# Kernel optimization log

Hardware: AMD Instinct MI355X
Metric: run time of the kernel (lower is better)

The kernel has to match this reference:

```python
import jax, jax.numpy as jnp
import numpy as np

HIDDEN = 768
NUM_LABELS = 25


def setup_inputs() -> dict:
    key = jax.random.key(0)
    k1, k2, k3, k4, k5 = jax.random.split(key, 5)
    B, H, S, E = 2, 12, 256, 64
    attention_probs = jax.random.uniform(k1, (B, H, S, S), dtype=jnp.float32)
    value_attentions = jax.random.normal(k2, (B, H, S, E), dtype=jnp.float32)
    relative_positions = jax.random.normal(k3, (B, S, S, H * E), dtype=jnp.float32)
    # nn.Linear(hidden_size, num_labels): weight [L, hidden], bias [L]
    bound = 1.0 / np.sqrt(HIDDEN)
    W = jax.random.uniform(k4, (NUM_LABELS, HIDDEN), dtype=jnp.float32, minval=-bound, maxval=bound)
    b = jax.random.uniform(k5, (NUM_LABELS,), dtype=jnp.float32, minval=-bound, maxval=bound)
    return {
        "attention_probs": attention_probs,
        "value_attentions": value_attentions,
        "relative_positions": relative_positions,
        "W": W,
        "b": b,
    }


def reference(attention_probs, value_attentions, relative_positions, W, b):
    B, H, S, E = value_attentions.shape
    # out[b,h,i,j,e] = probs[b,h,i,j] * (value[b,h,j,e] + rel[b,h,i,j,e])
    p = attention_probs[..., None]                      # [B,H,S,S,1]
    v = value_attentions[:, :, None, :, :]              # [B,H,1,S,E] broadcast over i
    rel = relative_positions.reshape(B, S, S, H, E).transpose(0, 3, 1, 2, 4)  # [B,H,S,S,E]
    out = p * (v + rel)                                 # [B,H,i,j,E]
    # permute(0,3,2,1,4) -> [B, j, i, H, E] -> [B,S,S,H*E]
    out = out.transpose(0, 3, 2, 1, 4).reshape(B, S, S, H * E)
    out = out @ W.T + b                                 # [B,S,S,L]
    return out.transpose(0, 1, 3, 2)                    # [B,S,L,S]
```

## Files before the change

### kernel.cpp

```cpp
#include <hip/hip_runtime.h>

#define NB 2
#define NH 12
#define NS 256
#define NE 64
#define NC 768
#define NL 25

__global__ __launch_bounds__(256) void tmhs_main(
    const float* __restrict__ p,
    const float* __restrict__ v,
    const float* __restrict__ rel,
    const float* __restrict__ W,
    const float* __restrict__ bias,
    float* __restrict__ out)
{
    __shared__ float sR[64][68];

    const int tid = threadIdx.x;
    const int bx  = blockIdx.x;
    const int it  = bx & 3;
    const int j   = (bx >> 2) & 255;
    const int b   = bx >> 10;
    const int i0  = it << 6;

    const int ig = tid & 63;
    const int wv = __builtin_amdgcn_readfirstlane(tid >> 6);
    const int l0 = wv * 6;

    float acc[7] = {0.f,0.f,0.f,0.f,0.f,0.f,0.f};

    const int row  = tid >> 2;
    const int part = tid & 3;

    for (int k = 0; k < NH; ++k) {
        __syncthreads();
        {
            const float  pr = p[((b*NH + k)*NS + (i0 + row))*NS + j];
            const float4* vp = (const float4*)(v + (((b*NH + k)*NS + j) << 6) + part*16);
            const float4* rs = (const float4*)(rel + ((b*NS + (i0+row))*NS + j)*NC + k*64 + part*16);
            float4* dst = (float4*)&sR[row][part*16];
#pragma unroll
            for (int q = 0; q < 4; ++q) {
                float4 a = rs[q];
                const float4 bb = vp[q];
                a.x = pr*(a.x + bb.x); a.y = pr*(a.y + bb.y);
                a.z = pr*(a.z + bb.z); a.w = pr*(a.w + bb.w);
                dst[q] = a;
            }
        }
        __syncthreads();

        const float* wk = W + k*64;
#pragma unroll
        for (int e4 = 0; e4 < 16; ++e4) {
            const float4 r4 = *(const float4*)&sR[ig][e4*4];
#pragma unroll
            for (int u = 0; u < 7; ++u) {
                const float4 w4 = *(const float4*)(wk + (l0 + u)*NC + e4*4);
                acc[u] = fmaf(r4.x, w4.x, acc[u]);
                acc[u] = fmaf(r4.y, w4.y, acc[u]);
                acc[u] = fmaf(r4.z, w4.z, acc[u]);
                acc[u] = fmaf(r4.w, w4.w, acc[u]);
            }
        }
    }

    const int ob = ((b*NS + j)*NL)*NS + i0 + ig;
#pragma unroll
    for (int u = 0; u < 7; ++u) {
        const int l = l0 + u;
        out[ob + l*NS] = acc[u] + bias[l];
    }
}

extern "C" void kernel_launch(void* const* d_in, const int* in_sizes, int n_in,
                              void* d_out, int out_size, void* d_ws, size_t ws_size,
                              hipStream_t stream) {
    const float* p    = (const float*)d_in[0];
    const float* v    = (const float*)d_in[1];
    const float* rel  = (const float*)d_in[2];
    const float* W    = (const float*)d_in[3];
    const float* bias = (const float*)d_in[4];
    float* out = (float*)d_out;
    tmhs_main<<<dim3(NB * NS * 4), dim3(256), 0, stream>>>(p, v, rel, W, bias, out);
}
```

Before: 612.0 us.

## Use bf16 MFMA for the label projection with a padded bf16 weight copy

Replaces the scalar FP32 FMA projection with bf16 MFMA 16x16x32 instructions. W is first converted to a zero-padded 32-row bf16 buffer in workspace by a separate prep kernel. The fused activations are packed to bf16 in shared memory, and the tiling changes to 128 i-rows per block over 128-wide K chunks. The kernel is dominated by the large rel stream, so compute savings may matter less, and bf16 lowers accuracy.

```diff
diff --git a/kernel.cpp b/kernel.cpp
--- a/kernel.cpp
+++ b/kernel.cpp
@@ -1,4 +1,5 @@
 #include <hip/hip_runtime.h>
+#include <hip/hip_bf16.h>
 
 #define NB 2
 #define NH 12
@@ -7,70 +8,108 @@
 #define NC 768
 #define NL 25
 
-__global__ __launch_bounds__(256) void tmhs_main(
+#define CH 128
+#define NCH 6
+#define TI 128
+#define SAS 132
+
+typedef __attribute__((ext_vector_type(8))) short short8;
+typedef __attribute__((ext_vector_type(4))) float float4v;
+
+__device__ __forceinline__ unsigned short bfb(float x) {
+    __hip_bfloat16 h = __float2bfloat16(x);
+    return *reinterpret_cast<unsigned short*>(&h);
+}
+__device__ __forceinline__ unsigned int pk2(float x, float y) {
+    return (unsigned int)bfb(x) | ((unsigned int)bfb(y) << 16);
+}
+
+__global__ void prep_w(const float* __restrict__ W, unsigned short* __restrict__ Wb) {
+    int idx = blockIdx.x * 256 + threadIdx.x;
+    if (idx >= 32 * NC) return;
+    int row = idx / NC;
+    int col = idx - row * NC;
+    Wb[idx] = (row < NL) ? bfb(W[row * NC + col]) : (unsigned short)0;
+}
+
+__global__ __launch_bounds__(256, 4) void tmhs_mfma(
     const float* __restrict__ p,
     const float* __restrict__ v,
     const float* __restrict__ rel,
-    const float* __restrict__ W,
+    const unsigned short* __restrict__ Wb,
     const float* __restrict__ bias,
     float* __restrict__ out)
 {
-    __shared__ float sR[64][68];
+    __shared__ unsigned short sA[TI][SAS];
 
     const int tid = threadIdx.x;
     const int bx  = blockIdx.x;
-    const int it  = bx & 3;
-    const int j   = (bx >> 2) & 255;
-    const int b   = bx >> 10;
-    const int i0  = it << 6;
+    const int ih  = bx & 1;
+    const int j   = (bx >> 1) & 255;
+    const int b   = bx >> 9;
+    const int i0  = ih * TI;
 
-    const int ig = tid & 63;
-    const int wv = __builtin_amdgcn_readfirstlane(tid >> 6);
-    const int l0 = wv * 6;
+    const int lane = tid & 63;
+    const int wv   = tid >> 6;
+    const int n15  = lane & 15;
+    const int quad = lane >> 4;
 
-    float acc[7] = {0.f,0.f,0.f,0.f,0.f,0.f,0.f};
+    float4v z = {0.f, 0.f, 0.f, 0.f};
+    float4v acc[2][2] = {{z, z}, {z, z}};
 
-    const int row  = tid >> 2;
-    const int part = tid & 3;
+    const int srow  = tid >> 1;
+    const int shalf = tid & 1;
 
-    for (int k = 0; k < NH; ++k) {
+    for (int ch = 0; ch < NCH; ++ch) {
+        const int kc = ch * CH;
+        const int h  = (kc >> 6) + shalf;
         __syncthreads();
         {
-            const float  pr = p[((b*NH + k)*NS + (i0 + row))*NS + j];
-            const float4* vp = (const float4*)(v + (((b*NH + k)*NS + j) << 6) + part*16);
-            const float4* rs = (const float4*)(rel + ((b*NS + (i0+row))*NS + j)*NC + k*64 + part*16);
-            float4* dst = (float4*)&sR[row][part*16];
+            const float  pr = p[((b*NH + h)*NS + (i0 + srow))*NS + j];
+            const float4* rs = (const float4*)(rel + ((b*NS + i0 + srow)*NS + j)*NC + kc + shalf*64);
+            const float4* vs = (const float4*)(v + ((b*NH + h)*NS + j)*NE);
+            unsigned int* dst = (unsigned int*)&sA[srow][shalf*64];
 #pragma unroll
-            for (int q = 0; q < 4; ++q) {
-                float4 a = rs[q];
-                const float4 bb = vp[q];
-                a.x = pr*(a.x + bb.x); a.y = pr*(a.y + bb.y);
-                a.z = pr*(a.z + bb.z); a.w = pr*(a.w + bb.w);
-                dst[q] = a;
+            for (int q = 0; q < 16; ++q) {
+                const float4 rr = rs[q];
+                const float4 vv = vs[q];
+                uint2 w2;
+                w2.x = pk2(pr*(rr.x+vv.x), pr*(rr.y+vv.y));
+                w2.y = pk2(pr*(rr.z+vv.z), pr*(rr.w+vv.w));
+                *(uint2*)(dst + q*2) = w2;
             }
         }
         __syncthreads();
 
-        const float* wk = W + k*64;
 #pragma unroll
-        for (int e4 = 0; e4 < 16; ++e4) {
-            const float4 r4 = *(const float4*)&sR[ig][e4*4];
+        for (int ks = 0; ks < 4; ++ks) {
+            short8 af0 = *(const short8*)(Wb + (     n15)*NC + kc + ks*32 + quad*8);
+            short8 af1 = *(const short8*)(Wb + (16 + n15)*NC + kc + ks*32 + quad*8);
 #pragma unroll
-            for (int u = 0; u < 7; ++u) {
-                const float4 w4 = *(const float4*)(wk + (l0 + u)*NC + e4*4);
-                acc[u] = fmaf(r4.x, w4.x, acc[u]);
-                acc[u] = fmaf(r4.y, w4.y, acc[u]);
-                acc[u] = fmaf(r4.z, w4.z, acc[u]);
-                acc[u] = fmaf(r4.w, w4.w, acc[u]);
+            for (int nt = 0; nt < 2; ++nt) {
+                const unsigned short* bp = &sA[wv*32 + nt*16 + n15][ks*32 + quad*8];
+                union { short8 s8; unsigned long long d[2]; } bu;
+                bu.d[0] = *(const unsigned long long*)bp;
+                bu.d[1] = *(const unsigned long long*)(bp + 4);
+                acc[0][nt] = __builtin_amdgcn_mfma_f32_16x16x32_bf16(af0, bu.s8, acc[0][nt], 0, 0, 0);
+                acc[1][nt] = __builtin_amdgcn_mfma_f32_16x16x32_bf16(af1, bu.s8, acc[1][nt], 0, 0, 0);
             }
         }
     }
 
-    const int ob = ((b*NS + j)*NL)*NS + i0 + ig;
+    const int obase = ((b*NS + j)*NL)*NS;
 #pragma unroll
-    for (int u = 0; u < 7; ++u) {
-        const int l = l0 + u;
-        out[ob + l*NS] = acc[u] + bias[l];
+    for (int nt = 0; nt < 2; ++nt) {
+        const int ii = i0 + wv*32 + nt*16 + n15;
+#pragma unroll
+        for (int mt = 0; mt < 2; ++mt) {
+#pragma unroll
+            for (int r = 0; r < 4; ++r) {
+                const int l = mt*16 + quad*4 + r;
+                if (l < NL)
+                    out[obase + l*NS + ii] = acc[mt][nt][r] + bias[l];
+            }
+        }
     }
 }
 
@@ -83,5 +122,8 @@
     const float* W    = (const float*)d_in[3];
     const float* bias = (const float*)d_in[4];
     float* out = (float*)d_out;
-    tmhs_main<<<dim3(NB * NS * 4), dim3(256), 0, stream>>>(p, v, rel, W, bias, out);
+    unsigned short* Wb = (unsigned short*)d_ws;
+
+    prep_w<<<dim3((32*NC + 255)/256), dim3(256), 0, stream>>>(W, Wb);
+    tmhs_mfma<<<dim3(NB * NS * 2), dim3(256), 0, stream>>>(p, v, rel, Wb, bias, out);
 }
```

Result: faster. 560.8 us (-8.4%).
